# Kernel optimization log

Hardware: AMD Instinct MI355X
Metric: run time of the kernel (lower is better)

Reference implementation:

```python
import jax, jax.numpy as jnp
import numpy as np

N, E = 50000, 800000
C_IN, C_OUT, HID = 64, 64, 64


def setup_inputs() -> dict:
    key = jax.random.key(0)
    ks = jax.random.split(key, 12)
    def rn(k, shape, scale=0.05):
        return jax.random.normal(k, shape, dtype=jnp.float32) * scale
    return dict(
        x=jax.random.normal(ks[0], (N, C_IN), dtype=jnp.float32),
        pos=jax.random.normal(ks[1], (N, 3), dtype=jnp.float32),
        edge_index=jax.random.randint(ks[2], (2, E), 0, N),
        W_in=rn(ks[3], (C_IN, C_IN)), b_in=jnp.zeros((C_IN,), jnp.float32),
        W_out=rn(ks[4], (C_OUT, C_OUT)), b_out=jnp.zeros((C_OUT,), jnp.float32),
        W_lin=rn(ks[5], (C_OUT, C_IN)),   # PointTransformerConv.lin (value), bias=False
        W_src=rn(ks[6], (C_OUT, C_IN)),   # lin_src, bias=False
        W_dst=rn(ks[7], (C_OUT, C_IN)),   # lin_dst, bias=False
        pos_w1=rn(ks[8], (HID, 3)), pos_b1=jnp.zeros((HID,), jnp.float32),
        pos_w2=rn(ks[9], (C_OUT, HID)), pos_b2=jnp.zeros((C_OUT,), jnp.float32),
        att_w1=rn(ks[10], (HID, C_OUT)), att_b1=jnp.zeros((HID,), jnp.float32),
        att_w2=rn(ks[11], (C_OUT, HID)), att_b2=jnp.zeros((C_OUT,), jnp.float32),
    )


def _mlp2(y, w1, b1, w2, b2):
    # MLP([a, 64, b], batch_norm=False): Linear->ReLU->Linear->ReLU
    y = jax.nn.relu(y @ w1.T + b1)
    return jax.nn.relu(y @ w2.T + b2)


def reference(x, pos, edge_index, W_in, b_in, W_out, b_out, W_lin, W_src, W_dst,
              pos_w1, pos_b1, pos_w2, pos_b2, att_w1, att_b1, att_w2, att_b2):
    n = x.shape[0]
    h = jax.nn.relu(x @ W_in.T + b_in)            # lin_in + relu, (N, C_in)
    v = h @ W_lin.T                                # value projection (N, C_out)
    k_src = h @ W_src.T                            # alpha_j source part
    q_dst = h @ W_dst.T                            # alpha_i dest part
    # PointTransformerConv adds self-loops by default
    loop = jnp.arange(n)
    src = jnp.concatenate([edge_index[0], loop])   # (E+N,)
    dst = jnp.concatenate([edge_index[1], loop])
    # per-edge positional encoding: pos_nn(pos_i - pos_j)
    delta = _mlp2(pos[dst] - pos[src], pos_w1, pos_b1, pos_w2, pos_b2)
    # per-edge attention logits: attn_nn(alpha_i - alpha_j), (E+N, C_out)
    alpha = _mlp2(q_dst[dst] - k_src[src], att_w1, att_b1, att_w2, att_b2)
    # per-destination-node channelwise softmax (self-loops ensure no empty segment)
    amax = jax.ops.segment_max(alpha, dst, num_segments=n)
    ex = jnp.exp(alpha - amax[dst])
    denom = jax.ops.segment_sum(ex, dst, num_segments=n)
    w = ex / (denom[dst] + 1e-16)
    # message = alpha * (x_j + delta); aggregate = sum over neighbors
    out = jax.ops.segment_sum(w * (v[src] + delta), dst, num_segments=n)
    return jax.nn.relu(out @ W_out.T + b_out)
```

## Files before the change

### kernel.cpp

```cpp
#include <hip/hip_runtime.h>
#include <math.h>

#define NN 50000
#define EE 800000
#define ET (EE + NN)
#define C  64
#define NBLK 49
#define NCHUNK 831
#define ZBLK 463

typedef __attribute__((ext_vector_type(8))) _Float16 f16x8;
typedef __attribute__((ext_vector_type(4))) _Float16 f16x4;
typedef __attribute__((ext_vector_type(2))) _Float16 f16x2;
typedef __attribute__((ext_vector_type(4))) float f32x4;

__device__ __forceinline__ f16x2 pk2(float a, float b) {
  return __builtin_bit_cast(f16x2, __builtin_amdgcn_cvt_pkrtz(a, b));
}
__device__ __forceinline__ f16x4 pk4(float a, float b, float c, float d) {
  return __builtin_shufflevector(pk2(a, b), pk2(c, d), 0, 1, 2, 3);
}
__device__ __forceinline__ f16x8 pk8(const float* y) {
  const f16x4 lo = pk4(y[0], y[1], y[2], y[3]);
  const f16x4 hi = pk4(y[4], y[5], y[6], y[7]);
  return __builtin_shufflevector(lo, hi, 0, 1, 2, 3, 4, 5, 6, 7);
}

__device__ __forceinline__ f16x8 frag_ldh(const _Float16* base, int row,
                                          int kofs) {
  return *(const f16x8*)(base + row * 72 + kofs);
}
__device__ __forceinline__ void stage_w(_Float16* __restrict__ dst,
                                        const _Float16* __restrict__ src16,
                                        int tid) {
  const f16x8* src = (const f16x8*)(src16 + tid * 16);
  _Float16* d = dst + (tid >> 2) * 72 + (tid & 3) * 16;
  ((f16x8*)d)[0] = src[0];
  ((f16x8*)d)[1] = src[1];
}

__device__ __forceinline__ int swzb(int row, int colbyte) {
  return row * 128 + (colbyte ^ ((row & 7) << 4));
}
__device__ __forceinline__ f16x8 frag_lds(const _Float16* base, int row,
                                          int kofs) {
  return *(const f16x8*)((const char*)base + swzb(row, kofs * 2));
}
__device__ __forceinline__ void stage_ws(_Float16* __restrict__ dst,
                                         const _Float16* __restrict__ src16,
                                         int tid) {
  const f16x8* src = (const f16x8*)(src16 + tid * 16);
  const int row = tid >> 2;
  const int c0 = (tid & 3) * 32;
  *(f16x8*)((char*)dst + swzb(row, c0)) = src[0];
  *(f16x8*)((char*)dst + swzb(row, c0 + 16)) = src[1];
}

__device__ __forceinline__ int psl(int e, int o) {
  return (e + 2 * o + (o >> 5)) & 63;
}

__global__ __launch_bounds__(256) void prep_kernel(
    const float* __restrict__ W_in, const float* __restrict__ W_lin,
    const float* __restrict__ W_src, const float* __restrict__ W_dst,
    const float* __restrict__ att_w1, const float* __restrict__ att_w2,
    const float* __restrict__ pos_w2, const float* __restrict__ W_out,
    _Float16* __restrict__ w16, int* __restrict__ cnt2) {
  if (blockIdx.x < 8) {
    const float* Ws[8] = {W_in, W_lin, W_src, W_dst, att_w1, att_w2, pos_w2,
                          W_out};
    const float* src = Ws[blockIdx.x];
    _Float16* dst = w16 + blockIdx.x * 4096;
    const float sc = (blockIdx.x == 5) ? 1.44269504088896340736f : 1.0f;
#pragma unroll
    for (int i = threadIdx.x * 4; i < 4096; i += 1024) {
      const float4 w = *(const float4*)(src + i);
      *(f16x4*)(dst + i) = pk4(w.x * sc, w.y * sc, w.z * sc, w.w * sc);
    }
  }
  int4* cz = (int4*)cnt2;
#pragma unroll 1
  for (int i = blockIdx.x * 256 + threadIdx.x; i < 2 * NN; i += 64 * 256)
    cz[i] = make_int4(0, 0, 0, 0);
}

__global__ __launch_bounds__(256) void scan_partial(const int* __restrict__ cnt2,
                                                    int* __restrict__ bsum,
                                                    float* __restrict__ zeroreg) {
  const int t = threadIdx.x;
  if (blockIdx.x >= NBLK) {
    const int zb = blockIdx.x - NBLK;
    float4* dst = (float4*)zeroreg;
    const int total4 = 2 * NN * 64 / 4;
    const float4 z = make_float4(0.f, 0.f, 0.f, 0.f);
#pragma unroll 1
    for (int i = zb * 256 + t; i < total4; i += ZBLK * 256) dst[i] = z;
    return;
  }
  __shared__ int ws[4];
  const int base = blockIdx.x * 1024 + t * 4;
  int s = 0;
  if (base + 3 < NN) {
#pragma unroll
    for (int sh = 0; sh < 8; ++sh) {
      const int4 v = *(const int4*)(cnt2 + sh * NN + base);
      s += v.x + v.y + v.z + v.w;
    }
  } else {
#pragma unroll
    for (int i = 0; i < 4; ++i)
      if (base + i < NN)
#pragma unroll
        for (int sh = 0; sh < 8; ++sh) s += cnt2[sh * NN + base + i];
  }
#pragma unroll
  for (int off = 32; off; off >>= 1) s += __shfl_down(s, off, 64);
  if ((t & 63) == 0) ws[t >> 6] = s;
  __syncthreads();
  if (t == 0) bsum[blockIdx.x] = ws[0] + ws[1] + ws[2] + ws[3];
}

__global__ __launch_bounds__(256) void scan_final(const int* __restrict__ cnt2,
                                                  const int* __restrict__ bsum,
                                                  int* __restrict__ curs2) {
  __shared__ int tsum[256];
  __shared__ int sblk[64];
  const int t = threadIdx.x;
  if (t < 64) {
    const int mine = (t < NBLK) ? bsum[t] : 0;
    int v = mine;
#pragma unroll
    for (int off = 1; off < 64; off <<= 1) {
      const int u = __shfl_up(v, off, 64);
      if (t >= off) v += u;
    }
    sblk[t] = v - mine;
  }
  const int base = blockIdx.x * 1024 + t * 4;
  int c2[8][4];
  int v[4] = {0, 0, 0, 0};
  if (base + 3 < NN) {
#pragma unroll
    for (int sh = 0; sh < 8; ++sh) {
      const int4 x = *(const int4*)(cnt2 + sh * NN + base);
      c2[sh][0] = x.x; c2[sh][1] = x.y; c2[sh][2] = x.z; c2[sh][3] = x.w;
      v[0] += x.x; v[1] += x.y; v[2] += x.z; v[3] += x.w;
    }
  } else {
#pragma unroll
    for (int sh = 0; sh < 8; ++sh)
#pragma unroll
      for (int i = 0; i < 4; ++i) {
        const int c = (base + i < NN) ? cnt2[sh * NN + base + i] : 0;
        c2[sh][i] = c;
        v[i] += c;
      }
  }
  const int s = v[0] + v[1] + v[2] + v[3];
  tsum[t] = s;
  __syncthreads();
  for (int off = 1; off < 256; off <<= 1) {
    const int u = (t >= off) ? tsum[t - off] : 0;
    __syncthreads();
    tsum[t] += u;
    __syncthreads();
  }
  int ex = sblk[blockIdx.x] + tsum[t] - s;
  int offs[8][4];
#pragma unroll
  for (int i = 0; i < 4; ++i) {
    int run = ex;
#pragma unroll
    for (int sh = 0; sh < 8; ++sh) {
      offs[sh][i] = run;
      run += c2[sh][i];
    }
    ex += v[i];
  }
  if (base + 3 < NN) {
#pragma unroll
    for (int sh = 0; sh < 8; ++sh)
      *(int4*)(curs2 + sh * NN + base) =
          make_int4(offs[sh][0], offs[sh][1], offs[sh][2], offs[sh][3]);
  } else {
#pragma unroll
    for (int sh = 0; sh < 8; ++sh)
#pragma unroll
      for (int i = 0; i < 4; ++i)
        if (base + i < NN) curs2[sh * NN + base + i] = offs[sh][i];
  }
}

__global__ __launch_bounds__(256) void scatter_kernel(const int* __restrict__ ei,
                                                      int* __restrict__ curs2,
                                                      int2* __restrict__ srt) {
  const int chunk = blockIdx.x;
  int* cs = curs2 + (chunk & 7) * NN;
  const int e0 = chunk * 1024 + threadIdx.x * 4;
  if (e0 >= ET) return;
  int s[4], d[4];
  if (e0 + 3 < EE) {
    const int4 sv = *(const int4*)(ei + e0);
    const int4 dv = *(const int4*)(ei + EE + e0);
    s[0] = sv.x; s[1] = sv.y; s[2] = sv.z; s[3] = sv.w;
    d[0] = dv.x; d[1] = dv.y; d[2] = dv.z; d[3] = dv.w;
  } else {
#pragma unroll
    for (int i = 0; i < 4; ++i) {
      const int e = e0 + i;
      if (e < EE) {
        s[i] = ei[e];
        d[i] = ei[EE + e];
      } else if (e < ET) {
        s[i] = d[i] = e - EE;
      } else {
        s[i] = d[i] = -1;
      }
    }
  }
#pragma unroll
  for (int i = 0; i < 4; ++i) {
    if (d[i] >= 0) {
      const int p = atomicAdd(&cs[d[i]], 1);
      srt[p] = make_int2(s[i], d[i]);
    }
  }
}

__global__ __launch_bounds__(256, 3) void node_proj(
    const float* __restrict__ x, const float* __restrict__ b_in,
    const _Float16* __restrict__ w16, const int* __restrict__ ei,
    int* __restrict__ cnt2, _Float16* __restrict__ vh,
    _Float16* __restrict__ kh, _Float16* __restrict__ qh) {
  __shared__ __align__(16) _Float16 wlds[4 * 4608];
  __shared__ __align__(16) _Float16 hlds[4608];
  __shared__ float biasv[64];

  const int tid = threadIdx.x;
  const int nb = blockIdx.x * 64;
  const int l15 = tid & 15;
  const int quad = (tid >> 4) & 3;
  const int wband = tid >> 6;
  const int nloc = wband * 16 + l15;
  const int gn = nb + nloc;

#pragma unroll 1
  for (int chunk = blockIdx.x; chunk < NCHUNK; chunk += gridDim.x) {
    int* cs = cnt2 + (chunk & 7) * NN;
    const int e0 = chunk * 1024 + tid * 4;
    if (e0 < ET) {
      int d[4];
      if (e0 + 3 < EE) {
        const int4 dv = *(const int4*)(ei + EE + e0);
        d[0] = dv.x; d[1] = dv.y; d[2] = dv.z; d[3] = dv.w;
      } else {
#pragma unroll
        for (int i = 0; i < 4; ++i) {
          const int e = e0 + i;
          d[i] = (e < EE) ? ei[EE + e] : ((e < ET) ? e - EE : -1);
        }
      }
#pragma unroll
      for (int i = 0; i < 4; ++i)
        if (d[i] >= 0) atomicAdd(&cs[d[i]], 1);
    }
  }

#pragma unroll
  for (int w = 0; w < 4; ++w) stage_w(wlds + w * 4608, w16 + w * 4096, tid);
  if (tid < 64) biasv[tid] = b_in[tid];

  f16x8 bfrag[2];
#pragma unroll
  for (int ks = 0; ks < 2; ++ks) {
    float y[8] = {0.f, 0.f, 0.f, 0.f, 0.f, 0.f, 0.f, 0.f};
    if (gn < NN) {
      const float4 a = *(const float4*)(x + (size_t)gn * 64 + ks * 32 + quad * 8);
      const float4 b = *(const float4*)(x + (size_t)gn * 64 + ks * 32 + quad * 8 + 4);
      y[0] = a.x; y[1] = a.y; y[2] = a.z; y[3] = a.w;
      y[4] = b.x; y[5] = b.y; y[6] = b.z; y[7] = b.w;
    }
    bfrag[ks] = pk8(y);
  }
  __syncthreads();

#pragma unroll
  for (int t = 0; t < 4; ++t) {
    f32x4 acc = {0.f, 0.f, 0.f, 0.f};
#pragma unroll
    for (int ks = 0; ks < 2; ++ks) {
      const f16x8 af = frag_ldh(wlds, t * 16 + l15, ks * 32 + quad * 8);
      acc = __builtin_amdgcn_mfma_f32_16x16x32_f16(af, bfrag[ks], acc, 0, 0, 0);
    }
    const int hb = t * 16 + quad * 4;
    *(f16x4*)(hlds + nloc * 72 + hb) =
        pk4(fmaxf(acc[0] + biasv[hb + 0], 0.f), fmaxf(acc[1] + biasv[hb + 1], 0.f),
            fmaxf(acc[2] + biasv[hb + 2], 0.f), fmaxf(acc[3] + biasv[hb + 3], 0.f));
  }
  __syncthreads();

  f16x8 hfrag[2];
#pragma unroll
  for (int ks = 0; ks < 2; ++ks)
    hfrag[ks] = frag_ldh(hlds, nloc, ks * 32 + quad * 8);

  _Float16* outs[3] = {vh, kh, qh};
#pragma unroll
  for (int p = 0; p < 3; ++p) {
    const _Float16* W = wlds + (p + 1) * 4608;
#pragma unroll
    for (int t = 0; t < 4; ++t) {
      f32x4 acc = {0.f, 0.f, 0.f, 0.f};
#pragma unroll
      for (int ks = 0; ks < 2; ++ks) {
        const f16x8 af = frag_ldh(W, t * 16 + l15, ks * 32 + quad * 8);
        acc = __builtin_amdgcn_mfma_f32_16x16x32_f16(af, hfrag[ks], acc, 0, 0, 0);
      }
      if (gn < NN) {
        *(f16x4*)(outs[p] + (size_t)gn * 64 + t * 16 + quad * 4) =
            pk4(acc[0], acc[1], acc[2], acc[3]);
      }
    }
  }
}

__global__ __launch_bounds__(256, 6) void edge_pass(
    const int2* __restrict__ srt, const float* __restrict__ pos,
    const _Float16* __restrict__ vh, const _Float16* __restrict__ kh,
    const _Float16* __restrict__ qh, const _Float16* __restrict__ w16,
    const float* __restrict__ att_b1, const float* __restrict__ att_b2,
    const float* __restrict__ pos_w1, const float* __restrict__ pos_b1,
    const float* __restrict__ pos_b2, float* __restrict__ num,
    float* __restrict__ den) {
  __shared__ __align__(16) _Float16 smem[12288];
  __shared__ __align__(16) float posw1T[3 * 64];
  __shared__ float b1s[64], b2s[64], pb1s[64], pb2s[64];
  __shared__ int dsts[64];

  _Float16* W1 = smem;
  _Float16* W2 = smem + 4096;
  _Float16* HP = smem + 8192;
  f16x2* pairb = (f16x2*)smem;

  const int tid = threadIdx.x;
  const int eb = blockIdx.x * 64;
  const int l15 = tid & 15;
  const int quad = (tid >> 4) & 3;
  const int wband = tid >> 6;
  const int eloc = wband * 16 + l15;

  int s_mine, d_mine;
  f16x8 bfrag[2];
  float dp0, dp1, dp2;
  {
    const int e = eb + eloc;
    int2 sd = make_int2(0, 0);
    int valid_d = -1;
    if (e < ET) {
      sd = srt[e];
      valid_d = sd.y;
    }
    s_mine = sd.x;
    d_mine = sd.y;
    if (quad == 0) dsts[eloc] = valid_d;
#pragma unroll
    for (int ks = 0; ks < 2; ++ks) {
      const f16x8 qv =
          *(const f16x8*)(qh + (size_t)d_mine * 64 + ks * 32 + quad * 8);
      const f16x8 kv =
          *(const f16x8*)(kh + (size_t)s_mine * 64 + ks * 32 + quad * 8);
      bfrag[ks] = qv - kv;
    }
    dp0 = pos[(size_t)d_mine * 3 + 0] - pos[(size_t)s_mine * 3 + 0];
    dp1 = pos[(size_t)d_mine * 3 + 1] - pos[(size_t)s_mine * 3 + 1];
    dp2 = pos[(size_t)d_mine * 3 + 2] - pos[(size_t)s_mine * 3 + 2];
  }

  stage_ws(W1, w16 + 4 * 4096, tid);
  stage_ws(W2, w16 + 5 * 4096, tid);
  if (tid < 64) {
    b1s[tid] = att_b1[tid];
    b2s[tid] = att_b2[tid] * 1.44269504088896340736f;
    pb1s[tid] = pos_b1[tid];
    pb2s[tid] = pos_b2[tid];
    posw1T[0 * 64 + tid] = pos_w1[tid * 3 + 0];
    posw1T[1 * 64 + tid] = pos_w1[tid * 3 + 1];
    posw1T[2 * 64 + tid] = pos_w1[tid * 3 + 2];
  }
  __syncthreads();

#pragma unroll
  for (int t = 0; t < 4; ++t) {
    f32x4 acc = {0.f, 0.f, 0.f, 0.f};
#pragma unroll
    for (int ks = 0; ks < 2; ++ks) {
      const f16x8 af = frag_lds(W1, t * 16 + l15, ks * 32 + quad * 8);
      acc = __builtin_amdgcn_mfma_f32_16x16x32_f16(af, bfrag[ks], acc, 0, 0, 0);
    }
    const int hb = t * 16 + quad * 4;
    *(f16x4*)((char*)HP + swzb(eloc, hb * 2)) =
        pk4(fmaxf(acc[0] + b1s[hb + 0], 0.f), fmaxf(acc[1] + b1s[hb + 1], 0.f),
            fmaxf(acc[2] + b1s[hb + 2], 0.f), fmaxf(acc[3] + b1s[hb + 3], 0.f));
  }

  f16x8 hpfrag[2];
#pragma unroll
  for (int ks = 0; ks < 2; ++ks) {
    float hv[8];
#pragma unroll
    for (int j = 0; j < 8; ++j) {
      const int i = ks * 32 + quad * 8 + j;
      float h = pb1s[i];
      h = fmaf(dp0, posw1T[i], h);
      h = fmaf(dp1, posw1T[64 + i], h);
      h = fmaf(dp2, posw1T[128 + i], h);
      hv[j] = fmaxf(h, 0.f);
    }
    hpfrag[ks] = pk8(hv);
  }

  float ex[16];
  {
    f16x8 hfrag[2];
#pragma unroll
    for (int ks = 0; ks < 2; ++ks)
      hfrag[ks] = frag_lds(HP, eloc, ks * 32 + quad * 8);
#pragma unroll
    for (int t = 0; t < 4; ++t) {
      f32x4 acc = {0.f, 0.f, 0.f, 0.f};
#pragma unroll
      for (int ks = 0; ks < 2; ++ks) {
        const f16x8 af = frag_lds(W2, t * 16 + l15, ks * 32 + quad * 8);
        acc = __builtin_amdgcn_mfma_f32_16x16x32_f16(af, hfrag[ks], acc, 0, 0, 0);
      }
      const int ob = t * 16 + quad * 4;
#pragma unroll
      for (int r = 0; r < 4; ++r)
        ex[t * 4 + r] = __builtin_exp2f(fmaxf(acc[r] + b2s[ob + r], 0.f));
    }
  }
  float vr[16];
#pragma unroll
  for (int t = 0; t < 4; ++t) {
    const f16x4 v4 = *(const f16x4*)(vh + (size_t)s_mine * 64 + t * 16 + quad * 4);
    vr[t * 4 + 0] = (float)v4[0];
    vr[t * 4 + 1] = (float)v4[1];
    vr[t * 4 + 2] = (float)v4[2];
    vr[t * 4 + 3] = (float)v4[3];
  }
  __syncthreads();

  stage_ws(HP, w16 + 6 * 4096, tid);
  __syncthreads();

  float del[16];
#pragma unroll
  for (int t = 0; t < 4; ++t) {
    f32x4 acc = {0.f, 0.f, 0.f, 0.f};
#pragma unroll
    for (int ks = 0; ks < 2; ++ks) {
      const f16x8 af = frag_lds(HP, t * 16 + l15, ks * 32 + quad * 8);
      acc = __builtin_amdgcn_mfma_f32_16x16x32_f16(af, hpfrag[ks], acc, 0, 0, 0);
    }
    const int ob = t * 16 + quad * 4;
#pragma unroll
    for (int r = 0; r < 4; ++r)
      del[t * 4 + r] = fmaxf(acc[r] + pb2s[ob + r], 0.f);
  }

#pragma unroll
  for (int t = 0; t < 4; ++t) {
#pragma unroll
    for (int r = 0; r < 4; ++r) {
      const int o = t * 16 + quad * 4 + r;
      const float e_ = ex[t * 4 + r];
      pairb[o * 64 + psl(eloc, o)] =
          pk2(e_ * (vr[t * 4 + r] + del[t * 4 + r]), e_);
    }
  }
  __syncthreads();

  {
    const int c = tid & 63;
    const int r = tid >> 6;
    float am = 0.f, ae = 0.f;
    int cur = -1;
#pragma unroll 1
    for (int t2 = 0; t2 < 16; ++t2) {
      const int el = r * 16 + t2;
      const int d = dsts[el];
      if (d != cur) {
        if (cur >= 0) {
          unsafeAtomicAdd(num + (size_t)cur * 64 + c, am);
          unsafeAtomicAdd(den + (size_t)cur * 64 + c, ae);
        }
        cur = d;
        am = 0.f;
        ae = 0.f;
      }
      if (d >= 0) {
        const f16x2 pe = pairb[c * 64 + psl(el, c)];
        am += (float)pe[0];
        ae += (float)pe[1];
      }
    }
    if (cur >= 0) {
      unsafeAtomicAdd(num + (size_t)cur * 64 + c, am);
      unsafeAtomicAdd(den + (size_t)cur * 64 + c, ae);
    }
  }
}

__global__ __launch_bounds__(256, 4) void out_proj(
    const float* __restrict__ num, const float* __restrict__ den,
    const _Float16* __restrict__ w16, const float* __restrict__ b_out,
    float* __restrict__ out) {
  __shared__ __align__(16) _Float16 wlds[4608];
  __shared__ float biasv[64];

  const int tid = threadIdx.x;
  const int nb = blockIdx.x * 64;
  const int l15 = tid & 15;
  const int quad = (tid >> 4) & 3;
  const int wband = tid >> 6;
  const int gn = nb + wband * 16 + l15;

  stage_w(wlds, w16 + 7 * 4096, tid);
  if (tid < 64) biasv[tid] = b_out[tid];

  f16x8 bfrag[2];
#pragma unroll
  for (int ks = 0; ks < 2; ++ks) {
    float y[8] = {0.f, 0.f, 0.f, 0.f, 0.f, 0.f, 0.f, 0.f};
    if (gn < NN) {
      const size_t base = (size_t)gn * 64 + ks * 32 + quad * 8;
      const float4 n0 = *(const float4*)(num + base);
      const float4 n1 = *(const float4*)(num + base + 4);
      const float4 d0 = *(const float4*)(den + base);
      const float4 d1 = *(const float4*)(den + base + 4);
      y[0] = n0.x / (d0.x + 1e-16f); y[1] = n0.y / (d0.y + 1e-16f);
      y[2] = n0.z / (d0.z + 1e-16f); y[3] = n0.w / (d0.w + 1e-16f);
      y[4] = n1.x / (d1.x + 1e-16f); y[5] = n1.y / (d1.y + 1e-16f);
      y[6] = n1.z / (d1.z + 1e-16f); y[7] = n1.w / (d1.w + 1e-16f);
    }
    bfrag[ks] = pk8(y);
  }
  __syncthreads();

#pragma unroll
  for (int t = 0; t < 4; ++t) {
    f32x4 acc = {0.f, 0.f, 0.f, 0.f};
#pragma unroll
    for (int ks = 0; ks < 2; ++ks) {
      const f16x8 af = frag_ldh(wlds, t * 16 + l15, ks * 32 + quad * 8);
      acc = __builtin_amdgcn_mfma_f32_16x16x32_f16(af, bfrag[ks], acc, 0, 0, 0);
    }
    if (gn < NN) {
      const int ob = t * 16 + quad * 4;
      float4 r;
      r.x = fmaxf(acc[0] + biasv[ob + 0], 0.f);
      r.y = fmaxf(acc[1] + biasv[ob + 1], 0.f);
      r.z = fmaxf(acc[2] + biasv[ob + 2], 0.f);
      r.w = fmaxf(acc[3] + biasv[ob + 3], 0.f);
      *(float4*)(out + (size_t)gn * 64 + ob) = r;
    }
  }
}

extern "C" void kernel_launch(void* const* d_in, const int* in_sizes, int n_in,
                              void* d_out, int out_size, void* d_ws,
                              size_t ws_size, hipStream_t stream) {
  const float* x      = (const float*)d_in[0];
  const float* pos    = (const float*)d_in[1];
  const int*   ei     = (const int*)d_in[2];
  const float* W_in   = (const float*)d_in[3];
  const float* b_in   = (const float*)d_in[4];
  const float* W_out  = (const float*)d_in[5];
  const float* b_out  = (const float*)d_in[6];
  const float* W_lin  = (const float*)d_in[7];
  const float* W_src  = (const float*)d_in[8];
  const float* W_dst  = (const float*)d_in[9];
  const float* pos_w1 = (const float*)d_in[10];
  const float* pos_b1 = (const float*)d_in[11];
  const float* pos_w2 = (const float*)d_in[12];
  const float* pos_b2 = (const float*)d_in[13];
  const float* att_w1 = (const float*)d_in[14];
  const float* att_b1 = (const float*)d_in[15];
  const float* att_w2 = (const float*)d_in[16];
  const float* att_b2 = (const float*)d_in[17];

  float* ws = (float*)d_ws;
  const size_t NC = (size_t)NN * C;
  float* num = ws;
  float* den = ws + NC;
  _Float16* vh = (_Float16*)(ws + 2 * NC);
  _Float16* kh = vh + NC;
  _Float16* qh = kh + NC;
  _Float16* w16 = qh + NC;
  int* ib     = (int*)(w16 + 8 * 4096);
  int* cnt2   = ib;
  int* curs2  = ib + 8 * NN;
  int* bsum   = ib + 16 * NN;
  int2* srt   = (int2*)(((uintptr_t)(bsum + NBLK) + 15) & ~(uintptr_t)15);

  const dim3 blk(256);
  prep_kernel<<<dim3(64), blk, 0, stream>>>(W_in, W_lin, W_src, W_dst, att_w1,
                                            att_w2, pos_w2, W_out, w16, cnt2);
  node_proj<<<dim3((NN + 63) / 64), blk, 0, stream>>>(x, b_in, w16, ei, cnt2,
                                                      vh, kh, qh);
  scan_partial<<<dim3(NBLK + ZBLK), blk, 0, stream>>>(cnt2, bsum, num);
  scan_final<<<dim3(NBLK), blk, 0, stream>>>(cnt2, bsum, curs2);
  scatter_kernel<<<dim3(NCHUNK), blk, 0, stream>>>(ei, curs2, srt);
  edge_pass<<<dim3((ET + 63) / 64), blk, 0, stream>>>(
      srt, pos, vh, kh, qh, w16, att_b1, att_b2, pos_w1, pos_b1, pos_b2, num,
      den);
  out_proj<<<dim3((NN + 63) / 64), blk, 0, stream>>>(num, den, w16, b_out,
                                                     (float*)d_out);
}
```

Baseline: 291.5 us.

## Shrink node_proj LDS with swizzle, add setprio around MFMA, stage pos deltas in LDS

node_proj drops padded LDS arrays and the bias LDS copy in favour of swizzled unpadded layouts and direct bias loads, and raises the launch-bounds occupancy target from 3 to 4. edge_pass brackets its MFMA loops with s_setprio, computes the position deltas only in quad-0 lanes and shares them through LDS as fp16 to cut redundant global loads and registers, and replaces the fp16-to-fp32 converts in the reduction with fdot2. The fp16 rounding of position deltas adds a little precision loss, and the extra LDS traffic and priority changes may not pay off.

```diff
diff --git a/kernel.cpp b/kernel.cpp
--- a/kernel.cpp
+++ b/kernel.cpp
@@ -227,14 +227,13 @@
   }
 }
 
-__global__ __launch_bounds__(256, 3) void node_proj(
+__global__ __launch_bounds__(256, 4) void node_proj(
     const float* __restrict__ x, const float* __restrict__ b_in,
     const _Float16* __restrict__ w16, const int* __restrict__ ei,
     int* __restrict__ cnt2, _Float16* __restrict__ vh,
     _Float16* __restrict__ kh, _Float16* __restrict__ qh) {
-  __shared__ __align__(16) _Float16 wlds[4 * 4608];
-  __shared__ __align__(16) _Float16 hlds[4608];
-  __shared__ float biasv[64];
+  __shared__ __align__(16) _Float16 wlds[4 * 4096];
+  __shared__ __align__(16) _Float16 hlds[4096];
 
   const int tid = threadIdx.x;
   const int nb = blockIdx.x * 64;
@@ -267,8 +266,7 @@
   }
 
 #pragma unroll
-  for (int w = 0; w < 4; ++w) stage_w(wlds + w * 4608, w16 + w * 4096, tid);
-  if (tid < 64) biasv[tid] = b_in[tid];
+  for (int w = 0; w < 4; ++w) stage_ws(wlds + w * 4096, w16 + w * 4096, tid);
 
   f16x8 bfrag[2];
 #pragma unroll
@@ -284,36 +282,39 @@
   }
   __syncthreads();
 
+  __builtin_amdgcn_s_setprio(1);
 #pragma unroll
   for (int t = 0; t < 4; ++t) {
     f32x4 acc = {0.f, 0.f, 0.f, 0.f};
 #pragma unroll
     for (int ks = 0; ks < 2; ++ks) {
-      const f16x8 af = frag_ldh(wlds, t * 16 + l15, ks * 32 + quad * 8);
+      const f16x8 af = frag_lds(wlds, t * 16 + l15, ks * 32 + quad * 8);
       acc = __builtin_amdgcn_mfma_f32_16x16x32_f16(af, bfrag[ks], acc, 0, 0, 0);
     }
     const int hb = t * 16 + quad * 4;
-    *(f16x4*)(hlds + nloc * 72 + hb) =
-        pk4(fmaxf(acc[0] + biasv[hb + 0], 0.f), fmaxf(acc[1] + biasv[hb + 1], 0.f),
-            fmaxf(acc[2] + biasv[hb + 2], 0.f), fmaxf(acc[3] + biasv[hb + 3], 0.f));
-  }
+    const float4 bv = *(const float4*)(b_in + hb);
+    *(f16x4*)((char*)hlds + swzb(nloc, hb * 2)) =
+        pk4(fmaxf(acc[0] + bv.x, 0.f), fmaxf(acc[1] + bv.y, 0.f),
+            fmaxf(acc[2] + bv.z, 0.f), fmaxf(acc[3] + bv.w, 0.f));
+  }
+  __builtin_amdgcn_s_setprio(0);
   __syncthreads();
 
   f16x8 hfrag[2];
 #pragma unroll
   for (int ks = 0; ks < 2; ++ks)
-    hfrag[ks] = frag_ldh(hlds, nloc, ks * 32 + quad * 8);
+    hfrag[ks] = frag_lds(hlds, nloc, ks * 32 + quad * 8);
 
   _Float16* outs[3] = {vh, kh, qh};
 #pragma unroll
   for (int p = 0; p < 3; ++p) {
-    const _Float16* W = wlds + (p + 1) * 4608;
+    const _Float16* W = wlds + (p + 1) * 4096;
 #pragma unroll
     for (int t = 0; t < 4; ++t) {
       f32x4 acc = {0.f, 0.f, 0.f, 0.f};
 #pragma unroll
       for (int ks = 0; ks < 2; ++ks) {
-        const f16x8 af = frag_ldh(W, t * 16 + l15, ks * 32 + quad * 8);
+        const f16x8 af = frag_lds(W, t * 16 + l15, ks * 32 + quad * 8);
         acc = __builtin_amdgcn_mfma_f32_16x16x32_f16(af, hfrag[ks], acc, 0, 0, 0);
       }
       if (gn < NN) {
@@ -336,6 +337,7 @@
   __shared__ __align__(16) float posw1T[3 * 64];
   __shared__ float b1s[64], b2s[64], pb1s[64], pb2s[64];
   __shared__ int dsts[64];
+  __shared__ _Float16 dph[3 * 64];
 
   _Float16* W1 = smem;
   _Float16* W2 = smem + 4096;
@@ -351,7 +353,6 @@
 
   int s_mine, d_mine;
   f16x8 bfrag[2];
-  float dp0, dp1, dp2;
   {
     const int e = eb + eloc;
     int2 sd = make_int2(0, 0);
@@ -362,7 +363,15 @@
     }
     s_mine = sd.x;
     d_mine = sd.y;
-    if (quad == 0) dsts[eloc] = valid_d;
+    if (quad == 0) {
+      dsts[eloc] = valid_d;
+      const float d0 = pos[(size_t)d_mine * 3 + 0] - pos[(size_t)s_mine * 3 + 0];
+      const float d1 = pos[(size_t)d_mine * 3 + 1] - pos[(size_t)s_mine * 3 + 1];
+      const float d2 = pos[(size_t)d_mine * 3 + 2] - pos[(size_t)s_mine * 3 + 2];
+      dph[0 * 64 + eloc] = (_Float16)d0;
+      dph[1 * 64 + eloc] = (_Float16)d1;
+      dph[2 * 64 + eloc] = (_Float16)d2;
+    }
 #pragma unroll
     for (int ks = 0; ks < 2; ++ks) {
       const f16x8 qv =
@@ -371,9 +380,6 @@
           *(const f16x8*)(kh + (size_t)s_mine * 64 + ks * 32 + quad * 8);
       bfrag[ks] = qv - kv;
     }
-    dp0 = pos[(size_t)d_mine * 3 + 0] - pos[(size_t)s_mine * 3 + 0];
-    dp1 = pos[(size_t)d_mine * 3 + 1] - pos[(size_t)s_mine * 3 + 1];
-    dp2 = pos[(size_t)d_mine * 3 + 2] - pos[(size_t)s_mine * 3 + 2];
   }
 
   stage_ws(W1, w16 + 4 * 4096, tid);
@@ -389,6 +395,7 @@
   }
   __syncthreads();
 
+  __builtin_amdgcn_s_setprio(1);
 #pragma unroll
   for (int t = 0; t < 4; ++t) {
     f32x4 acc = {0.f, 0.f, 0.f, 0.f};
@@ -402,7 +409,11 @@
         pk4(fmaxf(acc[0] + b1s[hb + 0], 0.f), fmaxf(acc[1] + b1s[hb + 1], 0.f),
             fmaxf(acc[2] + b1s[hb + 2], 0.f), fmaxf(acc[3] + b1s[hb + 3], 0.f));
   }
-
+  __builtin_amdgcn_s_setprio(0);
+
+  const float dp0 = (float)dph[0 * 64 + eloc];
+  const float dp1 = (float)dph[1 * 64 + eloc];
+  const float dp2 = (float)dph[2 * 64 + eloc];
   f16x8 hpfrag[2];
 #pragma unroll
   for (int ks = 0; ks < 2; ++ks) {
@@ -425,6 +436,7 @@
 #pragma unroll
     for (int ks = 0; ks < 2; ++ks)
       hfrag[ks] = frag_lds(HP, eloc, ks * 32 + quad * 8);
+    __builtin_amdgcn_s_setprio(1);
 #pragma unroll
     for (int t = 0; t < 4; ++t) {
       f32x4 acc = {0.f, 0.f, 0.f, 0.f};
@@ -438,6 +450,7 @@
       for (int r = 0; r < 4; ++r)
         ex[t * 4 + r] = __builtin_exp2f(fmaxf(acc[r] + b2s[ob + r], 0.f));
     }
+    __builtin_amdgcn_s_setprio(0);
   }
   float vr[16];
 #pragma unroll
@@ -454,6 +467,7 @@
   __syncthreads();
 
   float del[16];
+  __builtin_amdgcn_s_setprio(1);
 #pragma unroll
   for (int t = 0; t < 4; ++t) {
     f32x4 acc = {0.f, 0.f, 0.f, 0.f};
@@ -467,6 +481,7 @@
     for (int r = 0; r < 4; ++r)
       del[t * 4 + r] = fmaxf(acc[r] + pb2s[ob + r], 0.f);
   }
+  __builtin_amdgcn_s_setprio(0);
 
 #pragma unroll
   for (int t = 0; t < 4; ++t) {
@@ -483,6 +498,8 @@
   {
     const int c = tid & 63;
     const int r = tid >> 6;
+    const f16x2 c10 = {(_Float16)1.0f, (_Float16)0.0f};
+    const f16x2 c01 = {(_Float16)0.0f, (_Float16)1.0f};
     float am = 0.f, ae = 0.f;
     int cur = -1;
 #pragma unroll 1
@@ -500,8 +517,8 @@
       }
       if (d >= 0) {
         const f16x2 pe = pairb[c * 64 + psl(el, c)];
-        am += (float)pe[0];
-        ae += (float)pe[1];
+        am = __builtin_amdgcn_fdot2(pe, c10, am, false);
+        ae = __builtin_amdgcn_fdot2(pe, c01, ae, false);
       }
     }
     if (cur >= 0) {
```

Result: slower. 309.8 us (+6.3%).
